# Optimization experiments

Measured on AMD Instinct MI355X. Metric: run time of the kernel, lower is better.

The kernel has to match this reference:

```python
import jax, jax.numpy as jnp
import numpy as np

B, T, D = 4, 2048, 1024
RANK, FACTOR, SUB = 8, 64, 4
S = 4 * SUB  # 16


def construct_hamilton(A):
    # A: [rank, 4, sub, sub] -> [rank, 4*sub, 4*sub]
    r, i, j, k = A[:, 0], A[:, 1], A[:, 2], A[:, 3]
    return jnp.concatenate([
        jnp.concatenate([r, -i, -j, -k], axis=2),
        jnp.concatenate([i, r, -k, j], axis=2),
        jnp.concatenate([j, k, r, -i], axis=2),
        jnp.concatenate([k, -j, i, r], axis=2),
    ], axis=1)


def setup_inputs() -> dict:
    key = jax.random.key(0)
    k1, k2, k3 = jax.random.split(key, 3)
    x = jax.random.normal(k1, (B, T, D), dtype=jnp.float32)
    A = jax.random.normal(k2, (RANK, 4, SUB, SUB), dtype=jnp.float32)
    # orthogonal-ish init with (r+1)^-0.5 scaling, like the torch init
    fB = jax.random.normal(k3, (RANK, FACTOR, FACTOR), dtype=jnp.float32)
    q, _ = jnp.linalg.qr(fB)
    scale = (jnp.arange(RANK, dtype=jnp.float32) + 1.0) ** -0.5
    factors_B = q * scale[:, None, None]
    bias = jnp.zeros((D,), dtype=jnp.float32)
    return {"x": x, "A": A, "factors_B": factors_B, "bias": bias}


def reference(x, A, factors_B, bias):
    Bb, Tt, Dd = x.shape
    x_flat = x.reshape(-1, S, FACTOR)          # [N, s, i]
    H = construct_hamilton(A)                   # [r, k, s]
    wav = jnp.einsum('nsi,rji->rnsj', x_flat, factors_B)  # [r, N, s, j]
    out = jnp.einsum('rnsj,rks->nkj', wav, H)   # [N, k, j]
    return out.reshape(Bb, Tt, Dd) + bias
```

## Files before the change

kernel.cpp:

```cpp
#include <hip/hip_runtime.h>
#include <stdint.h>

#define RANKS 8
#define MDIM 8192
#define KDIM 1024
#define NDIM 1024
#define BM 128
#define BN 128
#define BK 64
#define NT (KDIM / BK)

typedef __bf16 bf16x8 __attribute__((ext_vector_type(8)));
typedef unsigned short u16x8 __attribute__((ext_vector_type(8)));
typedef float f32x4 __attribute__((ext_vector_type(4)));

__device__ __forceinline__ unsigned short f2bf(float f) {
  union { float f; uint32_t u; } v; v.f = f;
  uint32_t u = v.u;
  u += 0x7FFFu + ((u >> 16) & 1u);
  return (unsigned short)(u >> 16);
}

__constant__ int   c_comp[4][4] = {{0,1,2,3},{1,0,3,2},{2,3,0,1},{3,2,1,0}};
__constant__ float c_sign[4][4] = {{1.f,-1.f,-1.f,-1.f},
                                   {1.f, 1.f,-1.f, 1.f},
                                   {1.f, 1.f, 1.f,-1.f},
                                   {1.f,-1.f, 1.f, 1.f}};

__global__ void build_W(const float* __restrict__ A, const float* __restrict__ fB,
                        unsigned short* __restrict__ W) {
  int idx = blockIdx.x * 256 + threadIdx.x;
  int p  = idx >> 8;
  int q4 = (idx & 255) << 2;
  int k = p >> 6, j = p & 63;
  int kb = k >> 2, ks = k & 3;
  int s = q4 >> 6;
  int sb = s >> 2, ss = s & 3;
  int   comp = c_comp[kb][sb];
  float sgn  = c_sign[kb][sb];
  float o0 = 0.f, o1 = 0.f, o2 = 0.f, o3 = 0.f;
  int i0 = q4 & 63;
#pragma unroll
  for (int r = 0; r < RANKS; ++r) {
    float h = sgn * A[r * 64 + comp * 16 + ks * 4 + ss];
    const float* fb = fB + r * 4096 + j * 64 + i0;
    o0 += h * fb[0]; o1 += h * fb[1]; o2 += h * fb[2]; o3 += h * fb[3];
  }
  ushort4 st;
  st.x = f2bf(o0); st.y = f2bf(o1); st.z = f2bf(o2); st.w = f2bf(o3);
  *reinterpret_cast<ushort4*>(W + (size_t)p * KDIM + q4) = st;
}

__device__ __forceinline__ void gload16(const unsigned short* g, unsigned short* l) {
  __builtin_amdgcn_global_load_lds(
      (const __attribute__((address_space(1))) unsigned int*)(uintptr_t)g,
      (__attribute__((address_space(3))) unsigned int*)(uintptr_t)l,
      16, 0, 0);
}

__global__ __launch_bounds__(256, 2) void gemm_ham(
    const float* __restrict__ x, const unsigned short* __restrict__ W,
    const float* __restrict__ bias, float* __restrict__ out) {
  __shared__ unsigned short Asm_[2][BM * BK];
  __shared__ unsigned short Bsm_[2][BN * BK];
  const int tid  = threadIdx.x;
  const int lane = tid & 63;
  const int wid  = tid >> 6;
  const int wr = wid >> 1, wc = wid & 1;

  const int flat = blockIdx.x;
  const int xa = flat & 7, xb = (flat >> 3) & 7, xc = flat >> 6;
  const int bx = xa * 8 + xb;
  const int by = xc;
  const int row0 = bx * BM;
  const int col0 = by * BN;

  f32x4 acc[4][4];
  f32x4 zero = {0.f, 0.f, 0.f, 0.f};
#pragma unroll
  for (int m = 0; m < 4; ++m)
#pragma unroll
    for (int n = 0; n < 4; ++n) acc[m][n] = zero;

  float4 ar[4][2];

  auto loadA = [&](int kt) {
    const int k0 = kt * BK;
#pragma unroll
    for (int g = 0; g < 4; ++g) {
      int idx8 = g * 256 + tid;
      int row = idx8 >> 3, col8 = (idx8 & 7) << 3;
      const float* src = x + (size_t)(row0 + row) * KDIM + k0 + col8;
      ar[g][0] = *reinterpret_cast<const float4*>(src);
      ar[g][1] = *reinterpret_cast<const float4*>(src + 4);
    }
  };
  auto writeA = [&](int b) {
#pragma unroll
    for (int g = 0; g < 4; ++g) {
      int idx8 = g * 256 + tid;
      int row = idx8 >> 3, col8 = (idx8 & 7) << 3;
      bf16x8 v;
      v[0] = (__bf16)ar[g][0].x; v[1] = (__bf16)ar[g][0].y;
      v[2] = (__bf16)ar[g][0].z; v[3] = (__bf16)ar[g][0].w;
      v[4] = (__bf16)ar[g][1].x; v[5] = (__bf16)ar[g][1].y;
      v[6] = (__bf16)ar[g][1].z; v[7] = (__bf16)ar[g][1].w;
      *reinterpret_cast<bf16x8*>(&Asm_[b][row * BK + col8]) = v;
    }
  };
  auto stageB = [&](int b, int k0) {
#pragma unroll
    for (int c = 0; c < 4; ++c) {
      int eo = c * 2048 + tid * 8;
      int rr = eo >> 6, cc = eo & 63;
      gload16(W + (size_t)(col0 + rr) * KDIM + k0 + cc, &Bsm_[b][eo]);
    }
  };

  loadA(0);
  writeA(0);
  stageB(0, 0);
  __syncthreads();

  int cur = 0;
  const int rb   = lane & 15;
  const int krd0 = (lane >> 4) * 8;
#pragma unroll 1
  for (int kt = 0; kt < NT; ++kt) {
    const bool next = (kt + 1 < NT);
    if (next) {
      loadA(kt + 1);
      stageB(cur ^ 1, (kt + 1) * BK);
    }
#pragma unroll
    for (int kk = 0; kk < 2; ++kk) {
      const int krd = kk * 32 + krd0;
      bf16x8 af[4], bfr[4];
#pragma unroll
      for (int m = 0; m < 4; ++m)
        af[m] = __builtin_bit_cast(bf16x8,
            *reinterpret_cast<const u16x8*>(&Asm_[cur][(wr * 64 + m * 16 + rb) * BK + krd]));
#pragma unroll
      for (int n = 0; n < 4; ++n)
        bfr[n] = __builtin_bit_cast(bf16x8,
            *reinterpret_cast<const u16x8*>(&Bsm_[cur][(wc * 64 + n * 16 + rb) * BK + krd]));
#pragma unroll
      for (int m = 0; m < 4; ++m)
#pragma unroll
        for (int n = 0; n < 4; ++n)
          acc[m][n] = __builtin_amdgcn_mfma_f32_16x16x32_bf16(af[m], bfr[n], acc[m][n], 0, 0, 0);
    }
    if (next) writeA(cur ^ 1);
    __syncthreads();
    cur ^= 1;
  }

  const int crow = row0 + wr * 64 + (lane >> 4) * 4;
  const int ccol = col0 + wc * 64 + (lane & 15);
#pragma unroll
  for (int n = 0; n < 4; ++n) {
    int c = ccol + n * 16;
    float bv = bias[c];
#pragma unroll
    for (int m = 0; m < 4; ++m)
#pragma unroll
      for (int v = 0; v < 4; ++v)
        out[(size_t)(crow + m * 16 + v) * NDIM + c] = acc[m][n][v] + bv;
  }
}

__global__ void fallback_kernel(const float* __restrict__ x, const float* __restrict__ A,
                                const float* __restrict__ fB, const float* __restrict__ bias,
                                float* __restrict__ out) {
  __shared__ float xrow[1024];
  const int n = blockIdx.x;
  const int tid = threadIdx.x;
  for (int t = tid; t < 1024; t += 256) xrow[t] = x[(size_t)n * 1024 + t];
  __syncthreads();
  for (int pp = 0; pp < 4; ++pp) {
    int p = pp * 256 + tid;
    int k = p >> 6, j = p & 63;
    int kb = k >> 2, ks = k & 3;
    float accv = 0.f;
    for (int s = 0; s < 16; ++s) {
      int sb = s >> 2, ss = s & 3;
      int comp = c_comp[kb][sb];
      float sgn = c_sign[kb][sb];
      float hA[RANKS];
#pragma unroll
      for (int r = 0; r < RANKS; ++r) hA[r] = sgn * A[r * 64 + comp * 16 + ks * 4 + ss];
      for (int i = 0; i < 64; ++i) {
        float w = 0.f;
#pragma unroll
        for (int r = 0; r < RANKS; ++r) w += hA[r] * fB[r * 4096 + j * 64 + i];
        accv += xrow[s * 64 + i] * w;
      }
    }
    out[(size_t)n * 1024 + p] = accv + bias[p];
  }
}

extern "C" void kernel_launch(void* const* d_in, const int* in_sizes, int n_in,
                              void* d_out, int out_size, void* d_ws, size_t ws_size,
                              hipStream_t stream) {
  const float* x    = (const float*)d_in[0];
  const float* A    = (const float*)d_in[1];
  const float* fB   = (const float*)d_in[2];
  const float* bias = (const float*)d_in[3];
  float* out = (float*)d_out;

  const size_t needW = (size_t)NDIM * KDIM * sizeof(unsigned short);
  if (ws_size >= needW) {
    unsigned short* W = (unsigned short*)d_ws;
    build_W<<<dim3(1024), dim3(256), 0, stream>>>(A, fB, W);
    gemm_ham<<<dim3((MDIM / BM) * (NDIM / BN)), dim3(256), 0, stream>>>(x, W, bias, out);
  } else {
    fallback_kernel<<<dim3(MDIM), dim3(256), 0, stream>>>(x, A, fB, bias, out);
  }
}
```

Baseline: 40.54 us.

## Deepen GEMM pipeline with triple-buffered B, swizzled LDS, 256-row tiles

```diff
diff --git a/kernel.cpp b/kernel.cpp
--- a/kernel.cpp
+++ b/kernel.cpp
@@ -5,10 +5,11 @@
 #define MDIM 8192
 #define KDIM 1024
 #define NDIM 1024
-#define BM 128
+#define BM 256
 #define BN 128
 #define BK 64
 #define NT (KDIM / BK)
+#define THREADS 512
 
 typedef __bf16 bf16x8 __attribute__((ext_vector_type(8)));
 typedef unsigned short u16x8 __attribute__((ext_vector_type(8)));
@@ -58,20 +59,26 @@
       16, 0, 0);
 }
 
-__global__ __launch_bounds__(256, 2) void gemm_ham(
+#define SWZ(r, cbyte) (((r) * 128) + ((cbyte) ^ (((r) & 7) << 4)))
+
+__global__ __launch_bounds__(THREADS, 2) void gemm_ham(
     const float* __restrict__ x, const unsigned short* __restrict__ W,
     const float* __restrict__ bias, float* __restrict__ out) {
   __shared__ unsigned short Asm_[2][BM * BK];
-  __shared__ unsigned short Bsm_[2][BN * BK];
+  __shared__ unsigned short Bsm_[3][BN * BK];
+
   const int tid  = threadIdx.x;
   const int lane = tid & 63;
   const int wid  = tid >> 6;
-  const int wr = wid >> 1, wc = wid & 1;
+  const int wr   = wid >> 1;
+  const int wc   = wid & 1;
+  const int rb   = lane & 15;
+  const int qtr  = lane >> 4;
 
   const int flat = blockIdx.x;
-  const int xa = flat & 7, xb = (flat >> 3) & 7, xc = flat >> 6;
-  const int bx = xa * 8 + xb;
-  const int by = xc;
+  const int xg = flat & 7, ig = flat >> 3;
+  const int bx = xg * 4 + (ig >> 3);
+  const int by = ig & 7;
   const int row0 = bx * BM;
   const int col0 = by * BN;
 
@@ -82,81 +89,114 @@
 #pragma unroll
     for (int n = 0; n < 4; ++n) acc[m][n] = zero;
 
-  float4 ar[4][2];
-
-  auto loadA = [&](int kt) {
+  float4 arE[8], arO[8];
+
+  auto loadA = [&](int kt, float4 (&ar)[8]) {
     const int k0 = kt * BK;
 #pragma unroll
     for (int g = 0; g < 4; ++g) {
-      int idx8 = g * 256 + tid;
-      int row = idx8 >> 3, col8 = (idx8 & 7) << 3;
-      const float* src = x + (size_t)(row0 + row) * KDIM + k0 + col8;
-      ar[g][0] = *reinterpret_cast<const float4*>(src);
-      ar[g][1] = *reinterpret_cast<const float4*>(src + 4);
-    }
-  };
-  auto writeA = [&](int b) {
+      int id = g * 512 + tid;
+      int r = id >> 3, c8 = (id & 7) << 3;
+      const float* src = x + (size_t)(row0 + r) * KDIM + k0 + c8;
+      ar[2 * g]     = *reinterpret_cast<const float4*>(src);
+      ar[2 * g + 1] = *reinterpret_cast<const float4*>(src + 4);
+    }
+  };
+  auto writeA = [&](unsigned short* dst, const float4 (&ar)[8]) {
 #pragma unroll
     for (int g = 0; g < 4; ++g) {
-      int idx8 = g * 256 + tid;
-      int row = idx8 >> 3, col8 = (idx8 & 7) << 3;
+      int id = g * 512 + tid;
+      int r = id >> 3, c8 = (id & 7) << 3;
       bf16x8 v;
-      v[0] = (__bf16)ar[g][0].x; v[1] = (__bf16)ar[g][0].y;
-      v[2] = (__bf16)ar[g][0].z; v[3] = (__bf16)ar[g][0].w;
-      v[4] = (__bf16)ar[g][1].x; v[5] = (__bf16)ar[g][1].y;
-      v[6] = (__bf16)ar[g][1].z; v[7] = (__bf16)ar[g][1].w;
-      *reinterpret_cast<bf16x8*>(&Asm_[b][row * BK + col8]) = v;
-    }
-  };
-  auto stageB = [&](int b, int k0) {
-#pragma unroll
-    for (int c = 0; c < 4; ++c) {
-      int eo = c * 2048 + tid * 8;
-      int rr = eo >> 6, cc = eo & 63;
-      gload16(W + (size_t)(col0 + rr) * KDIM + k0 + cc, &Bsm_[b][eo]);
-    }
-  };
-
-  loadA(0);
-  writeA(0);
-  stageB(0, 0);
-  __syncthreads();
-
-  int cur = 0;
-  const int rb   = lane & 15;
-  const int krd0 = (lane >> 4) * 8;
-#pragma unroll 1
-  for (int kt = 0; kt < NT; ++kt) {
-    const bool next = (kt + 1 < NT);
-    if (next) {
-      loadA(kt + 1);
-      stageB(cur ^ 1, (kt + 1) * BK);
-    }
+      v[0] = (__bf16)ar[2*g].x;   v[1] = (__bf16)ar[2*g].y;
+      v[2] = (__bf16)ar[2*g].z;   v[3] = (__bf16)ar[2*g].w;
+      v[4] = (__bf16)ar[2*g+1].x; v[5] = (__bf16)ar[2*g+1].y;
+      v[6] = (__bf16)ar[2*g+1].z; v[7] = (__bf16)ar[2*g+1].w;
+      *reinterpret_cast<bf16x8*>(
+          reinterpret_cast<char*>(dst) + SWZ(r, c8 * 2)) = v;
+    }
+  };
+  auto stageB = [&](int kt, int slot) {
+    unsigned short* dst = &Bsm_[slot][0];
+#pragma unroll
+    for (int g = 0; g < 2; ++g) {
+      int id = g * 512 + tid;
+      int r = id >> 3, ct = id & 7;
+      gload16(W + (size_t)(col0 + r) * KDIM + kt * BK + ((ct ^ (r & 7)) << 3),
+              dst + id * 8);
+    }
+  };
+
+  auto tile = [&](int t, const unsigned short* Ard, unsigned short* Awr,
+                  float4 (&arLd)[8], float4 (&arWr)[8], int scur, int sstage) {
+    const bool doStage = (t + 2 < NT);
+    const bool doWrite = (t + 1 < NT);
+    if (doStage) {
+      loadA(t + 2, arLd);
+      stageB(t + 2, sstage);
+    }
+    __builtin_amdgcn_sched_barrier(0);
+    const unsigned short* Brd = &Bsm_[0][0] + scur * (BN * BK);
+    __builtin_amdgcn_s_setprio(1);
 #pragma unroll
     for (int kk = 0; kk < 2; ++kk) {
-      const int krd = kk * 32 + krd0;
+      const int cb = (qtr * 8 + kk * 32) * 2;
       bf16x8 af[4], bfr[4];
 #pragma unroll
-      for (int m = 0; m < 4; ++m)
-        af[m] = __builtin_bit_cast(bf16x8,
-            *reinterpret_cast<const u16x8*>(&Asm_[cur][(wr * 64 + m * 16 + rb) * BK + krd]));
-#pragma unroll
-      for (int n = 0; n < 4; ++n)
-        bfr[n] = __builtin_bit_cast(bf16x8,
-            *reinterpret_cast<const u16x8*>(&Bsm_[cur][(wc * 64 + n * 16 + rb) * BK + krd]));
+      for (int m = 0; m < 4; ++m) {
+        int r = wr * 64 + m * 16 + rb;
+        af[m] = *reinterpret_cast<const bf16x8*>(
+            reinterpret_cast<const char*>(Ard) + SWZ(r, cb));
+      }
+#pragma unroll
+      for (int n = 0; n < 4; ++n) {
+        int r = wc * 64 + n * 16 + rb;
+        bfr[n] = *reinterpret_cast<const bf16x8*>(
+            reinterpret_cast<const char*>(Brd) + SWZ(r, cb));
+      }
 #pragma unroll
       for (int m = 0; m < 4; ++m)
 #pragma unroll
         for (int n = 0; n < 4; ++n)
           acc[m][n] = __builtin_amdgcn_mfma_f32_16x16x32_bf16(af[m], bfr[n], acc[m][n], 0, 0, 0);
     }
-    if (next) writeA(cur ^ 1);
-    __syncthreads();
-    cur ^= 1;
-  }
-
-  const int crow = row0 + wr * 64 + (lane >> 4) * 4;
-  const int ccol = col0 + wc * 64 + (lane & 15);
+    __builtin_amdgcn_s_setprio(0);
+    if (doWrite) writeA(Awr, arWr);
+    __builtin_amdgcn_sched_barrier(0);
+    if (t < NT - 1) {
+      if (doStage) asm volatile("s_waitcnt vmcnt(10)" ::: "memory");
+      else         asm volatile("s_waitcnt vmcnt(0)"  ::: "memory");
+      asm volatile("s_waitcnt lgkmcnt(0)" ::: "memory");
+      __builtin_amdgcn_sched_barrier(0);
+      __builtin_amdgcn_s_barrier();
+      __builtin_amdgcn_sched_barrier(0);
+    }
+  };
+
+  loadA(0, arE);
+  writeA(&Asm_[0][0], arE);
+  stageB(0, 0);
+  loadA(1, arO);
+  stageB(1, 1);
+  asm volatile("s_waitcnt vmcnt(10)" ::: "memory");
+  asm volatile("s_waitcnt lgkmcnt(0)" ::: "memory");
+  __builtin_amdgcn_sched_barrier(0);
+  __builtin_amdgcn_s_barrier();
+  __builtin_amdgcn_sched_barrier(0);
+
+  int sc = 0;
+#pragma unroll 1
+  for (int t2 = 0; t2 < NT; t2 += 2) {
+    int ss0 = (sc == 0) ? 2 : sc - 1;
+    tile(t2, &Asm_[0][0], &Asm_[1][0], arE, arO, sc, ss0);
+    sc = (sc == 2) ? 0 : sc + 1;
+    int ss1 = (sc == 0) ? 2 : sc - 1;
+    tile(t2 + 1, &Asm_[1][0], &Asm_[0][0], arO, arE, sc, ss1);
+    sc = (sc == 2) ? 0 : sc + 1;
+  }
+
+  const int crow = row0 + wr * 64 + qtr * 4;
+  const int ccol = col0 + wc * 64 + rb;
 #pragma unroll
   for (int n = 0; n < 4; ++n) {
     int c = ccol + n * 16;
@@ -213,7 +253,7 @@
   if (ws_size >= needW) {
     unsigned short* W = (unsigned short*)d_ws;
     build_W<<<dim3(1024), dim3(256), 0, stream>>>(A, fB, W);
-    gemm_ham<<<dim3((MDIM / BM) * (NDIM / BN)), dim3(256), 0, stream>>>(x, W, bias, out);
+    gemm_ham<<<dim3((MDIM / BM) * (NDIM / BN)), dim3(THREADS), 0, stream>>>(x, W, bias, out);
   } else {
     fallback_kernel<<<dim3(MDIM), dim3(256), 0, stream>>>(x, A, fB, bias, out);
   }
```

After: 36.51 us. 9.9% less time.
